# Performance work log

Hardware: AMD Instinct MI355X
Metric: run time of the kernel (lower is better)

The kernel has to match this reference:

```python
import jax, jax.numpy as jnp
import numpy as np

B, N, D = 8, 1024, 1024
H, DQK, DV = 8, 128, 128
L, TB = 2, 128
LN_EPS = 1e-6
LOG2 = 0.69314718056


def _layer_norm(x, g, b):
    mu = jnp.mean(x, axis=-1, keepdims=True)
    var = jnp.mean(jnp.square(x - mu), axis=-1, keepdims=True)
    return (x - mu) * jax.lax.rsqrt(var + LN_EPS) * g + b


def setup_inputs() -> dict:
    key = jax.random.key(0)
    ks = jax.random.split(key, 8)
    x = 0.02 * jax.random.normal(ks[0], (B, N, D), dtype=jnp.float32)
    timestamps = jnp.sort(jax.random.randint(ks[1], (B, N), 0, 10_000_000), axis=1).astype(jnp.int64)
    lengths = jax.random.randint(ks[2], (B,), N // 4, N + 1)
    mask = (jnp.arange(N)[None, :] < lengths[:, None]).astype(jnp.float32)  # ragged prefix mask
    return {
        "x": x,
        "timestamps": timestamps,
        "mask": mask,
        "ln1_g": jnp.ones((L, D), jnp.float32),
        "ln1_b": jnp.zeros((L, D), jnp.float32),
        "w_uvqk": 0.02 * jax.random.normal(ks[3], (L, D, 2 * H * DV + 2 * H * DQK), jnp.float32),
        "b_uvqk": jnp.zeros((L, 2 * H * DV + 2 * H * DQK), jnp.float32),
        "ln2_g": jnp.ones((L, H * DV), jnp.float32),
        "ln2_b": jnp.zeros((L, H * DV), jnp.float32),
        "w_o": 0.02 * jax.random.normal(ks[4], (L, H * DV, D), jnp.float32),
        "b_o": jnp.zeros((L, D), jnp.float32),
        "pos_w": 0.02 * jax.random.normal(ks[5], (2 * N - 1,), jnp.float32),
        "ts_w": 0.02 * jax.random.normal(ks[6], (TB + 1,), jnp.float32),
    }


def _forward(x, timestamps, mask, ln1_g, ln1_b, w_uvqk, b_uvqk, ln2_g, ln2_b, w_o, b_o, pos_w, ts_w):
    # relative position bias: pos_w[(n - m) + N - 1]
    i = jnp.arange(N)
    rel_pos = pos_w[jnp.clip(i[:, None] - i[None, :] + N - 1, 0, 2 * N - 2)]  # [N, N]
    # bucketized relative time bias (log2 bucketization, detached indices)
    ext = jnp.concatenate([timestamps, timestamps[:, -1:]], axis=1)  # [B, N+1]
    delta = ext[:, 1:, None] - ext[:, None, :-1]  # [B, N, N]
    bucket = jnp.clip(
        (jnp.log(jnp.clip(jnp.abs(delta).astype(jnp.float32), 1.0, None)) / LOG2).astype(jnp.int32),
        0, TB)
    rab = rel_pos[None, :, :] + ts_w[bucket]  # [B, N, N]
    # causal * key-validity mask (invalid_attn_mask = 1 - triu; jagged padding is zero)
    amask = jnp.tril(jnp.ones((N, N), x.dtype))[None] * mask[:, None, :]  # [B, N, N]
    x = x * mask[..., None]
    for l in range(L):
        h = _layer_norm(x, ln1_g[l], ln1_b[l])
        uvqk = jax.nn.silu(h @ w_uvqk[l] + b_uvqk[l])  # [B, N, 4096]
        u = uvqk[..., : H * DV]
        v = uvqk[..., H * DV: 2 * H * DV].reshape(B, N, H, DV)
        q = uvqk[..., 2 * H * DV: 2 * H * DV + H * DQK].reshape(B, N, H, DQK)
        k = uvqk[..., 2 * H * DV + H * DQK:].reshape(B, N, H, DQK)
        attn = jax.nn.silu(jnp.einsum('bnhd,bmhd->bhnm', q, k) + rab[:, None]) / N
        attn = attn * amask[:, None]
        o = jnp.einsum('bhnm,bmhd->bnhd', attn, v).reshape(B, N, H * DV)
        x = x + (_layer_norm(o, ln2_g[l], ln2_b[l]) * u) @ w_o[l] + b_o[l]
    # F.normalize(p=2)
    ue = x / jnp.clip(jnp.linalg.norm(x, axis=-1, keepdims=True), 1e-12)
    lengths = mask.sum(axis=1).astype(jnp.int32)  # [B]
    last = ue[jnp.arange(B), lengths - 1]  # gather last valid token, [B, D]
    avg = (ue * mask[..., None]).sum(axis=1) / lengths[:, None].astype(ue.dtype)
    pooled = 0.5 * (last + avg)
    pooled = pooled / jnp.clip(jnp.linalg.norm(pooled, axis=-1, keepdims=True), 1e-12)
    return pooled


def reference(x, timestamps, mask, ln1_g, ln1_b, w_uvqk, b_uvqk, ln2_g, ln2_b, w_o, b_o, pos_w, ts_w):
    return _forward(x, timestamps, mask, ln1_g, ln1_b, w_uvqk, b_uvqk, ln2_g, ln2_b, w_o, b_o, pos_w, ts_w)
```

## Files before the change

kernel.cpp:

```cpp
#include <hip/hip_runtime.h>
#include <hip/hip_bf16.h>
#include <cstdint>
#include <cstddef>


#define BB   8
#define NNN  1024
#define DDD  1024
#define HHH  8
#define DVV  128
#define CCC  4096
#define TBK  128

typedef __bf16 bf8_t  __attribute__((ext_vector_type(8)));
typedef float  f4_t   __attribute__((ext_vector_type(4)));

__device__ __forceinline__ float bf2f(ushort u) {
  union { uint i; float f; } v; v.i = ((uint)u) << 16; return v.f;
}
__device__ __forceinline__ ushort f2bf(float f) {
  __hip_bfloat16 h = __float2bfloat16(f);
  return *(ushort*)&h;
}

__device__ __forceinline__ float block_reduce_sum(float v, float* sm) {
#pragma unroll
  for (int o = 32; o > 0; o >>= 1) v += __shfl_down(v, o, 64);
  int lane = threadIdx.x & 63;
  int wid  = threadIdx.x >> 6;
  __syncthreads();
  if (lane == 0) sm[wid] = v;
  __syncthreads();
  int nw = blockDim.x >> 6;
  float r = (threadIdx.x < nw) ? sm[threadIdx.x] : 0.f;
#pragma unroll
  for (int o = 8; o > 0; o >>= 1) r += __shfl_down(r, o, 64);
  if (threadIdx.x == 0) sm[0] = r;
  __syncthreads();
  return sm[0];
}

__global__ __launch_bounds__(256) void mask_x_k(const float* __restrict__ x,
                                                const float* __restrict__ mask,
                                                float* __restrict__ xb) {
  size_t i4 = (size_t)blockIdx.x * 256 + threadIdx.x;
  size_t row = i4 >> 8;
  float m = mask[row];
  float4 v = ((const float4*)x)[i4];
  v.x *= m; v.y *= m; v.z *= m; v.w *= m;
  ((float4*)xb)[i4] = v;
}

__global__ __launch_bounds__(256) void wconv_k(const float* __restrict__ W,
                                               ushort* __restrict__ Wt,
                                               int K, int Nn) {
  __shared__ float t[32][33];
  int k0 = blockIdx.x * 32, n0 = blockIdx.y * 32;
  int tx = threadIdx.x & 31, ty = threadIdx.x >> 5;
  for (int r = ty; r < 32; r += 8)
    t[r][tx] = W[(size_t)(k0 + r) * Nn + n0 + tx];
  __syncthreads();
  for (int r = ty; r < 32; r += 8)
    Wt[(size_t)(n0 + r) * K + k0 + tx] = f2bf(t[tx][r]);
}

__global__ __launch_bounds__(256) void rab_k(const int* __restrict__ ts,
                                             const float* __restrict__ pos_w,
                                             const float* __restrict__ ts_w,
                                             ushort* __restrict__ rabb) {
  int jt = blockIdx.x, it = blockIdx.y, b = blockIdx.z;
  if (jt > it) return;
  int j = jt * 128 + (threadIdx.x & 127);
  int half = threadIdx.x >> 7;
  int tsj = ts[(size_t)b * NNN + j];
  for (int rr = 0; rr < 64; ++rr) {
    int i = it * 128 + rr * 2 + half;
    int ii = i + 1; if (ii > NNN - 1) ii = NNN - 1;
    int tsi = ts[(size_t)b * NNN + ii];
    float af = fabsf((float)(tsi - tsj));
    af = fmaxf(af, 1.f);
    int bkt = (int)__log2f(af);
    bkt = min(max(bkt, 0), TBK);
    float rab = pos_w[i - j + NNN - 1] + ts_w[bkt];
    rabb[((size_t)b * NNN + i) * NNN + j] = f2bf(rab);
  }
}

__global__ __launch_bounds__(256) void ln_k(const float* __restrict__ X,
                                            const float* __restrict__ g,
                                            const float* __restrict__ bsh,
                                            const float* __restrict__ umat,
                                            int ustride,
                                            ushort* __restrict__ Y) {
  __shared__ float sm[16];
  size_t row = blockIdx.x;
  const float* xr = X + row * DDD;
  int d = threadIdx.x * 4;
  float4 xv = *(const float4*)(xr + d);
  float s = xv.x + xv.y + xv.z + xv.w;
  s = block_reduce_sum(s, sm);
  float mu = s * (1.f / 1024.f);
  float d0 = xv.x - mu, d1 = xv.y - mu, d2 = xv.z - mu, d3 = xv.w - mu;
  float ss = d0 * d0 + d1 * d1 + d2 * d2 + d3 * d3;
  ss = block_reduce_sum(ss, sm);
  float rs = rsqrtf(ss * (1.f / 1024.f) + 1e-6f);
  float y0 = d0 * rs * g[d + 0] + bsh[d + 0];
  float y1 = d1 * rs * g[d + 1] + bsh[d + 1];
  float y2 = d2 * rs * g[d + 2] + bsh[d + 2];
  float y3 = d3 * rs * g[d + 3] + bsh[d + 3];
  if (umat != nullptr) {
    const float* ur = umat + row * (size_t)ustride + d;
    y0 *= ur[0]; y1 *= ur[1]; y2 *= ur[2]; y3 *= ur[3];
  }
  ushort tmp[4] = { f2bf(y0), f2bf(y1), f2bf(y2), f2bf(y3) };
  *(uint2*)(Y + row * DDD + d) = *(uint2*)tmp;
}

template <int MODE>
__global__ __launch_bounds__(256) void gemm_bf_k(const ushort* __restrict__ A,
                                                 const ushort* __restrict__ Bt,
                                                 const float* __restrict__ bias,
                                                 float* __restrict__ C,
                                                 ushort* __restrict__ Cb,
                                                 int K, int Nn) {
  __shared__ alignas(16) ushort As[128 * 32];
  __shared__ alignas(16) ushort Bs[128 * 32];
  int tid = threadIdx.x;
  int wave = tid >> 6, lane = tid & 63;
  int quad = lane >> 4, l16 = lane & 15;
  int wm = wave >> 1, wn = wave & 1;
  int m0 = blockIdx.y * 128, n0 = blockIdx.x * 128;

  f4_t acc[4][4] = {};

  int r_l = tid >> 2;
  int p   = tid & 3;

  for (int k0 = 0; k0 < K; k0 += 32) {
    __syncthreads();
#pragma unroll
    for (int g = 0; g < 2; ++g) {
      int row = g * 64 + r_l;
      int q = (p - (row >> 1)) & 3;
      __builtin_amdgcn_global_load_lds(
          (const __attribute__((address_space(1))) void*)(A + (size_t)(m0 + row) * K + k0 + q * 8),
          (__attribute__((address_space(3))) void*)(As + (g * 64 + wave * 16) * 32),
          16, 0, 0);
      __builtin_amdgcn_global_load_lds(
          (const __attribute__((address_space(1))) void*)(Bt + (size_t)(n0 + row) * K + k0 + q * 8),
          (__attribute__((address_space(3))) void*)(Bs + (g * 64 + wave * 16) * 32),
          16, 0, 0);
    }
    __syncthreads();

    bf8_t af[4], bfr[4];
#pragma unroll
    for (int t = 0; t < 4; ++t) {
      int row = wm * 64 + t * 16 + l16;
      af[t] = *(const bf8_t*)&As[row * 32 + ((quad + (row >> 1)) & 3) * 8];
      int col = wn * 64 + t * 16 + l16;
      bfr[t] = *(const bf8_t*)&Bs[col * 32 + ((quad + (col >> 1)) & 3) * 8];
    }
#pragma unroll
    for (int i = 0; i < 4; ++i)
#pragma unroll
      for (int j = 0; j < 4; ++j)
        acc[i][j] = __builtin_amdgcn_mfma_f32_16x16x32_bf16(af[i], bfr[j],
                                                            acc[i][j], 0, 0, 0);
  }

#pragma unroll
  for (int j = 0; j < 4; ++j) {
    int col = n0 + wn * 64 + j * 16 + l16;
    float bz = bias[col];
#pragma unroll
    for (int i = 0; i < 4; ++i) {
      int rbase = m0 + wm * 64 + i * 16 + quad * 4;
#pragma unroll
      for (int r = 0; r < 4; ++r) {
        float z = acc[i][j][r] + bz;
        int row = rbase + r;
        if (MODE == 1) {
          C[(size_t)row * Nn + col] += z;
        } else {
          float s = z / (1.f + __expf(-z));
          if (col < 1024) C[(size_t)row * 1024 + col] = s;
          else Cb[(size_t)row * 3072 + (col - 1024)] = f2bf(s);
        }
      }
    }
  }
}

__global__ __launch_bounds__(256) void vt_k(const ushort* __restrict__ qkv,
                                            ushort* __restrict__ vt) {
  __shared__ ushort t[32][33];
  int bh = blockIdx.z; int b = bh >> 3, h = bh & 7;
  int nt = blockIdx.x * 32, dt = blockIdx.y * 32;
  int tx = threadIdx.x & 31, ty = threadIdx.x >> 5;
  for (int rr = ty; rr < 32; rr += 8)
    t[rr][tx] = qkv[(size_t)(b * NNN + nt + rr) * 3072 + h * 128 + dt + tx];
  __syncthreads();
  for (int rr = ty; rr < 32; rr += 8)
    vt[((size_t)bh * 128 + dt + rr) * NNN + nt + tx] = t[tx][rr];
}

__global__ __launch_bounds__(256, 4) void attn_mfma_k(
    const ushort* __restrict__ qkv, const ushort* __restrict__ vt,
    const ushort* __restrict__ rabb, const float* __restrict__ mask,
    float* __restrict__ o) {
  __shared__ alignas(16) ushort Ks[64 * 128];
  __shared__ alignas(16) ushort Vs[128 * 64];
  __shared__ alignas(16) ushort Ps[64 * 64];
  int h = blockIdx.y, b = blockIdx.z;
  int qt = ((int)blockIdx.x + (int)blockIdx.y + 2 * (int)blockIdx.z) & 15;
  int n0 = qt * 64;
  int tid = threadIdx.x, w = tid >> 6, lane = tid & 63;
  int quad = lane >> 4, l16 = lane & 15;

  const ushort* qg0 = qkv + ((size_t)(b * NNN + n0)) * 3072 + 1024 + h * 128;
#pragma unroll
  for (int t = 0; t < 4; ++t) {
    int lrow = w * 16 + t * 4 + (lane >> 4);
    int q = ((lane & 15) - lrow) & 15;
    __builtin_amdgcn_global_load_lds(
        (const __attribute__((address_space(1))) void*)(qg0 + (size_t)lrow * 3072 + q * 8),
        (__attribute__((address_space(3))) void*)(Ks + (w * 16 + t * 4) * 128),
        16, 0, 0);
  }
  __syncthreads();
  bf8_t qf[4];
  {
    int lr = w * 16 + l16;
#pragma unroll
    for (int kk = 0; kk < 4; ++kk)
      qf[kk] = *(const bf8_t*)&Ks[lr * 128 + (((kk * 4 + quad) + lr) & 15) * 8];
  }

  f4_t oacc[8] = {};
  const ushort* kg0 = qkv + (size_t)b * NNN * 3072 + 2048 + h * 128;
  const ushort* vg0 = vt + (size_t)(b * 8 + h) * 128 * NNN;
  const ushort* rb0 = rabb + ((size_t)(b * NNN + n0 + w * 16 + quad * 4)) * NNN;
  const float* mk0 = mask + (size_t)b * NNN;
  int mtmax = qt + 1;

  for (int mt = 0; mt < mtmax; ++mt) {
    int m0 = mt * 64;
    __syncthreads();
#pragma unroll
    for (int t = 0; t < 4; ++t) {
      int lrow = w * 16 + t * 4 + (lane >> 4);
      int q = ((lane & 15) - lrow) & 15;
      __builtin_amdgcn_global_load_lds(
          (const __attribute__((address_space(1))) void*)(kg0 + (size_t)(m0 + lrow) * 3072 + q * 8),
          (__attribute__((address_space(3))) void*)(Ks + (w * 16 + t * 4) * 128),
          16, 0, 0);
    }
#pragma unroll
    for (int t = 0; t < 4; ++t) {
      int dv = w * 32 + t * 8 + (lane >> 3);
      int q = ((lane & 7) - dv) & 7;
      __builtin_amdgcn_global_load_lds(
          (const __attribute__((address_space(1))) void*)(vg0 + (size_t)dv * NNN + m0 + q * 8),
          (__attribute__((address_space(3))) void*)(Vs + (w * 32 + t * 8) * 64),
          16, 0, 0);
    }
    ushort rv[4][4];
#pragma unroll
    for (int tj = 0; tj < 4; ++tj)
#pragma unroll
      for (int r = 0; r < 4; ++r)
        rv[tj][r] = rb0[(size_t)r * NNN + m0 + tj * 16 + l16];
    __syncthreads();

    f4_t sacc[4] = {};
#pragma unroll
    for (int kk = 0; kk < 4; ++kk) {
      bf8_t kf[4];
#pragma unroll
      for (int tj = 0; tj < 4; ++tj) {
        int lr = tj * 16 + l16;
        kf[tj] = *(const bf8_t*)&Ks[lr * 128 + (((kk * 4 + quad) + lr) & 15) * 8];
      }
#pragma unroll
      for (int tj = 0; tj < 4; ++tj)
        sacc[tj] = __builtin_amdgcn_mfma_f32_16x16x32_bf16(qf[kk], kf[tj],
                                                           sacc[tj], 0, 0, 0);
    }

#pragma unroll
    for (int tj = 0; tj < 4; ++tj) {
      int m = tj * 16 + l16;
      int gj = m0 + m;
      float msc = mk0[gj] * (1.f / 1024.f);
#pragma unroll
      for (int r = 0; r < 4; ++r) {
        int q = w * 16 + quad * 4 + r;
        int gi = n0 + q;
        float z = sacc[tj][r] + bf2f(rv[tj][r]);
        float pp = z / (1.f + __expf(-z)) * msc;
        if (gj > gi) pp = 0.f;
        Ps[q * 64 + (((m >> 3) + q) & 7) * 8 + (m & 7)] = f2bf(pp);
      }
    }

#pragma unroll
    for (int kk = 0; kk < 2; ++kk) {
      bf8_t pf, vf[8];
      {
        int q = w * 16 + l16;
        pf = *(const bf8_t*)&Ps[q * 64 + (((kk * 4 + quad) + q) & 7) * 8];
      }
#pragma unroll
      for (int tj = 0; tj < 8; ++tj) {
        int dv = tj * 16 + l16;
        vf[tj] = *(const bf8_t*)&Vs[dv * 64 + (((kk * 4 + quad) + dv) & 7) * 8];
      }
#pragma unroll
      for (int tj = 0; tj < 8; ++tj)
        oacc[tj] = __builtin_amdgcn_mfma_f32_16x16x32_bf16(pf, vf[tj],
                                                           oacc[tj], 0, 0, 0);
    }
  }

#pragma unroll
  for (int tj = 0; tj < 8; ++tj) {
    int col = h * 128 + tj * 16 + l16;
#pragma unroll
    for (int r = 0; r < 4; ++r) {
      int gi = n0 + w * 16 + quad * 4 + r;
      o[((size_t)(b * NNN + gi)) * DDD + col] = oacc[tj][r];
    }
  }
}

__global__ __launch_bounds__(256) void row_stats_k(const float* __restrict__ xb,
                                                   float* __restrict__ invn) {
  __shared__ float sm[16];
  size_t row = blockIdx.x;
  int d = threadIdx.x * 4;
  float4 xv = *(const float4*)(xb + row * DDD + d);
  float ss = xv.x * xv.x + xv.y * xv.y + xv.z * xv.z + xv.w * xv.w;
  ss = block_reduce_sum(ss, sm);
  if (threadIdx.x == 0) invn[row] = 1.f / fmaxf(sqrtf(ss), 1e-12f);
}

__global__ __launch_bounds__(1024) void pool_partial_k(const float* __restrict__ xb,
                                                       const float* __restrict__ mask,
                                                       const float* __restrict__ invn,
                                                       float* __restrict__ partial) {
  int b = blockIdx.x, c = blockIdx.y, d = threadIdx.x;
  float s = 0.f;
  int nbeg = c * 64;
  for (int n = nbeg; n < nbeg + 64; ++n) {
    size_t r = (size_t)b * NNN + n;
    s += xb[r * DDD + d] * mask[r] * invn[r];
  }
  partial[((size_t)b * 16 + c) * DDD + d] = s;
}

__global__ __launch_bounds__(1024) void pool_final_k(const float* __restrict__ xb,
                                                     const float* __restrict__ mask,
                                                     const float* __restrict__ invn,
                                                     const float* __restrict__ partial,
                                                     float* __restrict__ out) {
  __shared__ float sm[16];
  int b = blockIdx.x, d = threadIdx.x;
  float msum = mask[(size_t)b * NNN + d];
  msum = block_reduce_sum(msum, sm);
  int len = (int)(msum + 0.5f);
  float s = 0.f;
#pragma unroll
  for (int c = 0; c < 16; ++c) s += partial[((size_t)b * 16 + c) * DDD + d];
  float avg = s / (float)len;
  size_t lr = (size_t)b * NNN + (len - 1);
  float last = xb[lr * DDD + d] * invn[lr];
  float pooled = 0.5f * (last + avg);
  float ssq = block_reduce_sum(pooled * pooled, sm);
  out[(size_t)b * DDD + d] = pooled / fmaxf(sqrtf(ssq), 1e-12f);
}

extern "C" void kernel_launch(void* const* d_in, const int* in_sizes, int n_in,
                              void* d_out, int out_size, void* d_ws, size_t ws_size,
                              hipStream_t stream) {
  const float* x      = (const float*)d_in[0];
  const int*   ts     = (const int*)d_in[1];
  const float* mask   = (const float*)d_in[2];
  const float* ln1_g  = (const float*)d_in[3];
  const float* ln1_b  = (const float*)d_in[4];
  const float* w_uvqk = (const float*)d_in[5];
  const float* b_uvqk = (const float*)d_in[6];
  const float* ln2_g  = (const float*)d_in[7];
  const float* ln2_b  = (const float*)d_in[8];
  const float* w_o    = (const float*)d_in[9];
  const float* b_o    = (const float*)d_in[10];
  const float* pos_w  = (const float*)d_in[11];
  const float* ts_w   = (const float*)d_in[12];
  float* out = (float*)d_out;

  float* ws = (float*)d_ws;
  const size_t SZ = (size_t)BB * NNN * DDD;
  float* xb   = ws;
  float* buf1 = ws + SZ;
  float* ubuf = ws + 2 * SZ;
  ushort* hbf = (ushort*)(ws + 3 * SZ);
  ushort* wuT = hbf + SZ;
  ushort* woT = wuT + 2 * (size_t)DDD * CCC;
  ushort* qkvb = woT + 2 * (size_t)DDD * DDD;
  ushort* vtb  = qkvb + (size_t)BB * NNN * 3072;
  ushort* rabb = vtb + (size_t)BB * HHH * DVV * NNN;
  float* invn = (float*)(rabb + (size_t)BB * NNN * NNN);
  float* partial = invn + (size_t)BB * NNN;

  mask_x_k<<<(BB * NNN * DDD / 4) / 256, 256, 0, stream>>>(x, mask, xb);

  for (int l = 0; l < 2; ++l) {
    wconv_k<<<dim3(DDD / 32, CCC / 32), 256, 0, stream>>>(
        w_uvqk + (size_t)l * DDD * CCC, wuT + (size_t)l * CCC * DDD, DDD, CCC);
    wconv_k<<<dim3(DDD / 32, DDD / 32), 256, 0, stream>>>(
        w_o + (size_t)l * DDD * DDD, woT + (size_t)l * DDD * DDD, DDD, DDD);
  }

  rab_k<<<dim3(8, 8, BB), 256, 0, stream>>>(ts, pos_w, ts_w, rabb);

  for (int l = 0; l < 2; ++l) {
    ln_k<<<BB * NNN, 256, 0, stream>>>(xb, ln1_g + l * DDD, ln1_b + l * DDD,
                                       nullptr, 0, hbf);
    gemm_bf_k<2><<<dim3(CCC / 128, BB * NNN / 128), 256, 0, stream>>>(
        hbf, wuT + (size_t)l * CCC * DDD, b_uvqk + (size_t)l * CCC,
        ubuf, qkvb, DDD, CCC);
    vt_k<<<dim3(NNN / 32, DVV / 32, BB * HHH), 256, 0, stream>>>(qkvb, vtb);
    attn_mfma_k<<<dim3(NNN / 64, HHH, BB), 256, 0, stream>>>(
        qkvb, vtb, rabb, mask, buf1);
    ln_k<<<BB * NNN, 256, 0, stream>>>(buf1, ln2_g + l * DDD, ln2_b + l * DDD,
                                       ubuf, DDD, hbf);
    gemm_bf_k<1><<<dim3(DDD / 128, BB * NNN / 128), 256, 0, stream>>>(
        hbf, woT + (size_t)l * DDD * DDD, b_o + (size_t)l * DDD,
        xb, nullptr, DDD, DDD);
  }

  row_stats_k<<<BB * NNN, 256, 0, stream>>>(xb, invn);
  pool_partial_k<<<dim3(BB, 16), 1024, 0, stream>>>(xb, mask, invn, partial);
  pool_final_k<<<BB, 1024, 0, stream>>>(xb, mask, invn, partial, out);
}
```

Baseline: 734.3 us.

## Skip padded rows beyond sequence length across all kernels

Adds a small kernel that computes each batch's valid length from the prefix mask, then has the LN, GEMM, transpose, attention, rab, row-stats and pooling kernels return early for row tiles past that length. Padded query rows are masked out of attention keys and never feed the pooled output, so their computation is unnecessary. This relies on the mask being a contiguous prefix; padded rows keep stale or unwritten values in the workspace buffers.

```diff
diff --git a/kernel.cpp b/kernel.cpp
--- a/kernel.cpp
+++ b/kernel.cpp
@@ -38,6 +38,15 @@
   if (threadIdx.x == 0) sm[0] = r;
   __syncthreads();
   return sm[0];
+}
+
+__global__ __launch_bounds__(1024) void len_k(const float* __restrict__ mask,
+                                              int* __restrict__ lenp) {
+  __shared__ float sm[16];
+  int b = blockIdx.x;
+  float m = mask[(size_t)b * NNN + threadIdx.x];
+  float s = block_reduce_sum(m, sm);
+  if (threadIdx.x == 0) lenp[b] = (int)(s + 0.5f);
 }
 
 __global__ __launch_bounds__(256) void mask_x_k(const float* __restrict__ x,
@@ -67,9 +76,12 @@
 __global__ __launch_bounds__(256) void rab_k(const int* __restrict__ ts,
                                              const float* __restrict__ pos_w,
                                              const float* __restrict__ ts_w,
+                                             const int* __restrict__ lenp,
                                              ushort* __restrict__ rabb) {
   int jt = blockIdx.x, it = blockIdx.y, b = blockIdx.z;
   if (jt > it) return;
+  int len = lenp[b];
+  if (it * 128 >= len || jt * 128 >= len) return;
   int j = jt * 128 + (threadIdx.x & 127);
   int half = threadIdx.x >> 7;
   int tsj = ts[(size_t)b * NNN + j];
@@ -91,9 +103,11 @@
                                             const float* __restrict__ bsh,
                                             const float* __restrict__ umat,
                                             int ustride,
+                                            const int* __restrict__ lenp,
                                             ushort* __restrict__ Y) {
   __shared__ float sm[16];
   size_t row = blockIdx.x;
+  if (((int)row & 1023) >= lenp[row >> 10]) return;
   const float* xr = X + row * DDD;
   int d = threadIdx.x * 4;
   float4 xv = *(const float4*)(xr + d);
@@ -122,14 +136,16 @@
                                                  const float* __restrict__ bias,
                                                  float* __restrict__ C,
                                                  ushort* __restrict__ Cb,
+                                                 const int* __restrict__ lenp,
                                                  int K, int Nn) {
   __shared__ alignas(16) ushort As[128 * 32];
   __shared__ alignas(16) ushort Bs[128 * 32];
+  int m0 = blockIdx.y * 128, n0 = blockIdx.x * 128;
+  if ((m0 & 1023) >= lenp[m0 >> 10]) return;
   int tid = threadIdx.x;
   int wave = tid >> 6, lane = tid & 63;
   int quad = lane >> 4, l16 = lane & 15;
   int wm = wave >> 1, wn = wave & 1;
-  int m0 = blockIdx.y * 128, n0 = blockIdx.x * 128;
 
   f4_t acc[4][4] = {};
 
@@ -193,10 +209,12 @@
 }
 
 __global__ __launch_bounds__(256) void vt_k(const ushort* __restrict__ qkv,
+                                            const int* __restrict__ lenp,
                                             ushort* __restrict__ vt) {
   __shared__ ushort t[32][33];
   int bh = blockIdx.z; int b = bh >> 3, h = bh & 7;
   int nt = blockIdx.x * 32, dt = blockIdx.y * 32;
+  if (nt >= lenp[b]) return;
   int tx = threadIdx.x & 31, ty = threadIdx.x >> 5;
   for (int rr = ty; rr < 32; rr += 8)
     t[rr][tx] = qkv[(size_t)(b * NNN + nt + rr) * 3072 + h * 128 + dt + tx];
@@ -208,13 +226,14 @@
 __global__ __launch_bounds__(256, 4) void attn_mfma_k(
     const ushort* __restrict__ qkv, const ushort* __restrict__ vt,
     const ushort* __restrict__ rabb, const float* __restrict__ mask,
-    float* __restrict__ o) {
+    const int* __restrict__ lenp, float* __restrict__ o) {
   __shared__ alignas(16) ushort Ks[64 * 128];
   __shared__ alignas(16) ushort Vs[128 * 64];
   __shared__ alignas(16) ushort Ps[64 * 64];
   int h = blockIdx.y, b = blockIdx.z;
   int qt = ((int)blockIdx.x + (int)blockIdx.y + 2 * (int)blockIdx.z) & 15;
   int n0 = qt * 64;
+  if (n0 >= lenp[b]) return;
   int tid = threadIdx.x, w = tid >> 6, lane = tid & 63;
   int quad = lane >> 4, l16 = lane & 15;
 
@@ -335,9 +354,11 @@
 }
 
 __global__ __launch_bounds__(256) void row_stats_k(const float* __restrict__ xb,
+                                                   const int* __restrict__ lenp,
                                                    float* __restrict__ invn) {
   __shared__ float sm[16];
   size_t row = blockIdx.x;
+  if (((int)row & 1023) >= lenp[row >> 10]) return;
   int d = threadIdx.x * 4;
   float4 xv = *(const float4*)(xb + row * DDD + d);
   float ss = xv.x * xv.x + xv.y * xv.y + xv.z * xv.z + xv.w * xv.w;
@@ -348,27 +369,28 @@
 __global__ __launch_bounds__(1024) void pool_partial_k(const float* __restrict__ xb,
                                                        const float* __restrict__ mask,
                                                        const float* __restrict__ invn,
+                                                       const int* __restrict__ lenp,
                                                        float* __restrict__ partial) {
   int b = blockIdx.x, c = blockIdx.y, d = threadIdx.x;
+  int len = lenp[b];
   float s = 0.f;
   int nbeg = c * 64;
-  for (int n = nbeg; n < nbeg + 64; ++n) {
+  int nend = min(nbeg + 64, len);
+  for (int n = nbeg; n < nend; ++n) {
     size_t r = (size_t)b * NNN + n;
-    s += xb[r * DDD + d] * mask[r] * invn[r];
+    s += xb[r * DDD + d] * invn[r];
   }
   partial[((size_t)b * 16 + c) * DDD + d] = s;
 }
 
 __global__ __launch_bounds__(1024) void pool_final_k(const float* __restrict__ xb,
-                                                     const float* __restrict__ mask,
                                                      const float* __restrict__ invn,
                                                      const float* __restrict__ partial,
+                                                     const int* __restrict__ lenp,
                                                      float* __restrict__ out) {
   __shared__ float sm[16];
   int b = blockIdx.x, d = threadIdx.x;
-  float msum = mask[(size_t)b * NNN + d];
-  msum = block_reduce_sum(msum, sm);
-  int len = (int)(msum + 0.5f);
+  int len = lenp[b];
   float s = 0.f;
 #pragma unroll
   for (int c = 0; c < 16; ++c) s += partial[((size_t)b * 16 + c) * DDD + d];
@@ -411,8 +433,10 @@
   ushort* rabb = vtb + (size_t)BB * HHH * DVV * NNN;
   float* invn = (float*)(rabb + (size_t)BB * NNN * NNN);
   float* partial = invn + (size_t)BB * NNN;
+  int* lenp = (int*)(partial + (size_t)BB * 16 * DDD);
 
   mask_x_k<<<(BB * NNN * DDD / 4) / 256, 256, 0, stream>>>(x, mask, xb);
+  len_k<<<BB, 1024, 0, stream>>>(mask, lenp);
 
   for (int l = 0; l < 2; ++l) {
     wconv_k<<<dim3(DDD / 32, CCC / 32), 256, 0, stream>>>(
@@ -421,25 +445,25 @@
         w_o + (size_t)l * DDD * DDD, woT + (size_t)l * DDD * DDD, DDD, DDD);
   }
 
-  rab_k<<<dim3(8, 8, BB), 256, 0, stream>>>(ts, pos_w, ts_w, rabb);
+  rab_k<<<dim3(8, 8, BB), 256, 0, stream>>>(ts, pos_w, ts_w, lenp, rabb);
 
   for (int l = 0; l < 2; ++l) {
     ln_k<<<BB * NNN, 256, 0, stream>>>(xb, ln1_g + l * DDD, ln1_b + l * DDD,
-                                       nullptr, 0, hbf);
+                                       nullptr, 0, lenp, hbf);
     gemm_bf_k<2><<<dim3(CCC / 128, BB * NNN / 128), 256, 0, stream>>>(
         hbf, wuT + (size_t)l * CCC * DDD, b_uvqk + (size_t)l * CCC,
-        ubuf, qkvb, DDD, CCC);
-    vt_k<<<dim3(NNN / 32, DVV / 32, BB * HHH), 256, 0, stream>>>(qkvb, vtb);
+        ubuf, qkvb, lenp, DDD, CCC);
+    vt_k<<<dim3(NNN / 32, DVV / 32, BB * HHH), 256, 0, stream>>>(qkvb, lenp, vtb);
     attn_mfma_k<<<dim3(NNN / 64, HHH, BB), 256, 0, stream>>>(
-        qkvb, vtb, rabb, mask, buf1);
+        qkvb, vtb, rabb, mask, lenp, buf1);
     ln_k<<<BB * NNN, 256, 0, stream>>>(buf1, ln2_g + l * DDD, ln2_b + l * DDD,
-                                       ubuf, DDD, hbf);
+                                       ubuf, DDD, lenp, hbf);
     gemm_bf_k<1><<<dim3(DDD / 128, BB * NNN / 128), 256, 0, stream>>>(
         hbf, woT + (size_t)l * DDD * DDD, b_o + (size_t)l * DDD,
-        xb, nullptr, DDD, DDD);
-  }
-
-  row_stats_k<<<BB * NNN, 256, 0, stream>>>(xb, invn);
-  pool_partial_k<<<dim3(BB, 16), 1024, 0, stream>>>(xb, mask, invn, partial);
-  pool_final_k<<<BB, 1024, 0, stream>>>(xb, mask, invn, partial, out);
-}
+        xb, nullptr, lenp, DDD, DDD);
+  }
+
+  row_stats_k<<<BB * NNN, 256, 0, stream>>>(xb, lenp, invn);
+  pool_partial_k<<<dim3(BB, 16), 1024, 0, stream>>>(xb, mask, invn, lenp, partial);
+  pool_final_k<<<BB, 1024, 0, stream>>>(xb, invn, partial, lenp, out);
+}
```

New measurement: 704.0 us. 1.04x faster.
